# Optimization experiments

Measured on AMD Instinct MI355X. Metric: run time of the kernel, lower is better.

The kernel has to match this reference:

```python
import jax, jax.numpy as jnp
import numpy as np
from jax import lax

SIGMA, GAMMA, N_ORI = 6.0, 0.5, 6
WAVELENGTHS = (8.0, 10.0, 12.0)
KS = 37  # int(6*sigma)=36 -> +1 to make odd


def make_gabor_kernels():
    # Replicates cv2.getGaborKernel(psi=0); kernel is symmetric under 180-deg
    # rotation so cv2's index flip is a no-op and conv == correlation.
    half = KS // 2
    yy, xx = np.meshgrid(np.arange(-half, half + 1, dtype=np.float64),
                         np.arange(-half, half + 1, dtype=np.float64), indexing='ij')
    ks = []
    for lam in WAVELENGTHS:
        for t in range(N_ORI):
            th = t * np.pi / N_ORI
            xr = xx * np.cos(th) + yy * np.sin(th)
            yr = -xx * np.sin(th) + yy * np.cos(th)
            k = np.exp(-(xr ** 2 + (GAMMA ** 2) * yr ** 2) / (2.0 * SIGMA ** 2)) \
                * np.cos(2.0 * np.pi / lam * xr)
            ks.append(k.astype(np.float32))
    return jnp.asarray(np.stack(ks))[:, None]  # (F=18, 1, 37, 37)


def setup_inputs() -> dict:
    key = jax.random.key(0)
    x = jax.random.normal(key, (8, 3, 256, 256), dtype=jnp.float32)
    return {"x": x, "gabor_kernels": make_gabor_kernels()}


def haar_dwt2(x):
    # Single-level pywt haar dwt2; for even H,W symmetric padding never fires,
    # so each output pixel comes from a disjoint 2x2 block [[a,b],[c,d]].
    B, C, H, W = x.shape
    xb = x.reshape(B, C, H // 2, 2, W // 2, 2)
    a, b = xb[:, :, :, 0, :, 0], xb[:, :, :, 0, :, 1]
    c, d = xb[:, :, :, 1, :, 0], xb[:, :, :, 1, :, 1]
    LL = (a + b + c + d) * 0.5
    LH = (a + b - c - d) * 0.5  # pywt cH ('da'): high along rows
    HL = (a - b + c - d) * 0.5  # pywt cV ('ad'): high along cols
    HH = (a - b - c + d) * 0.5  # pywt cD ('dd')
    sub = jnp.stack([LL, LH, HL, HH], axis=2)  # (B, C, 4, H/2, W/2)
    return sub.reshape(B, C * 4, H // 2, W // 2)


def gabor_bank(x, kernels):
    # One grouped conv replaces the Python C x F conv2d loop. Group-major output
    # channel order (channel outer, filter inner) matches the torch loop order.
    B, C, H, W = x.shape
    F = kernels.shape[0]
    w = jnp.tile(kernels, (C, 1, 1, 1))  # (C*F, 1, KS, KS)
    pad = KS // 2
    return lax.conv_general_dilated(
        x, w, window_strides=(1, 1), padding=[(pad, pad), (pad, pad)],
        dimension_numbers=('NCHW', 'OIHW', 'NCHW'), feature_group_count=C)


def fft_channels(x):
    B, C, H, W = x.shape
    xc = jnp.fft.rfft2(x, norm='ortho')       # (B, C, H, W//2+1)
    mag = jnp.abs(xc)
    ph = jnp.arctan2(xc.imag, xc.real)        # torch.angle
    pad = W - mag.shape[-1]
    pads = [(0, 0), (0, 0), (0, 0), (0, pad)]
    return jnp.concatenate([jnp.pad(mag, pads), jnp.pad(ph, pads)], axis=1)


def reference(x, gabor_kernels):
    dwt = haar_dwt2(x)                 # (B, C*4, H/2, W/2)
    gab = gabor_bank(x, gabor_kernels)  # (B, C*18, H, W)
    fft = fft_channels(x)              # (B, C*2, H, W)
    return (dwt, gab, fft)
```

## Files before the change

### kernel.cpp

```cpp
#include <hip/hip_runtime.h>
#include <math.h>

#define BB 8
#define CC 3
#define HH 256
#define WW 256
#define KSZ 37
#define PD 18

#define DWT_OFF 0
#define GAB_OFF (8*12*128*128)
#define FFT_OFF (GAB_OFF + 8*54*256*256)

#define PSTRIDE 88

#define PREP_BLOCKS 888
#define FFTROW_BLOCKS 768
#define GAB_BLOCKS 1536
#define FFTCOL_BLOCKS 768

typedef short bf16x8 __attribute__((ext_vector_type(8)));
typedef float f32x16 __attribute__((ext_vector_type(16)));

__device__ __forceinline__ unsigned f2bf(float f) {
  unsigned u = __float_as_uint(f);
  return (u + 0x7fffu + ((u >> 16) & 1u)) >> 16;
}

__global__ __launch_bounds__(512) void fused_pre_kernel(
    const float* __restrict__ x, const float* __restrict__ wk,
    ushort* __restrict__ wshc, float* __restrict__ out) {
  __shared__ __align__(16) float smem[4352];
  const int g = blockIdx.x;
  const int tid = threadIdx.x;

  if (g < PREP_BLOCKS) {
    int idx = g * 512 + tid;
    int j = idx & 7; int rest = idx >> 3;
    int l = rest & 63; rest >>= 6;
    int t = rest % 3; rest /= 3;
    int ky = rest % 37; int s = rest / 37;
    int m = l & 31, hi = l >> 5;
    int kk = 16 * t + 8 * hi + j - s;
    float v = 0.0f;
    if (m < 18 && kk >= 0 && kk < 37) v = wk[(m * 37 + ky) * 37 + kk];
    wshc[idx] = (ushort)f2bf(v);
    return;
  }

  const int w = tid >> 6;
  const int t = tid & 63;
  const int rowid = (g - PREP_BLOCKS) * 8 + w;
  float* re  = smem + w * 256;
  float* im  = smem + 2048 + w * 256;
  float* twr = smem + 4096;
  float* twi = smem + 4224;

#pragma unroll
  for (int q = 0; q < 2; ++q) {
    int k = t + q * 64;
    float sn, cs;
    sincosf(-2.0f * (float)M_PI * (float)k / 256.0f, &sn, &cs);
    twr[k] = cs; twi[k] = sn;
  }

  const float* xr = x + (size_t)rowid * 256;
#pragma unroll
  for (int q = 0; q < 4; ++q) {
    int i = t + q * 64;
    int br = __brev((unsigned)i) >> 24;
    re[br] = xr[i];
    im[br] = 0.0f;
  }

  for (int s = 1; s <= 8; ++s) {
    int half = 1 << (s - 1);
    int sh = 8 - s;
#pragma unroll
    for (int q = 0; q < 2; ++q) {
      int j = t + q * 64;
      int gg = j >> (s - 1);
      int p = j & (half - 1);
      int i1 = (gg << s) + p;
      int i2 = i1 + half;
      float cs = twr[p << sh], sn = twi[p << sh];
      float r2 = re[i2], m2 = im[i2];
      float tr = r2 * cs - m2 * sn;
      float ti = r2 * sn + m2 * cs;
      float r1 = re[i1], m1 = im[i1];
      re[i2] = r1 - tr; im[i2] = m1 - ti;
      re[i1] = r1 + tr; im[i1] = m1 + ti;
    }
  }

  const int bc = rowid >> 8;
  const int y  = rowid & 255;
  const int b  = bc / 3, c = bc - b * 3;
  float* magrow = out + FFT_OFF + (size_t)(b * 6 + c) * (HH * WW) + (size_t)y * WW;
  float* phrow  = magrow + (size_t)3 * (HH * WW);
#pragma unroll
  for (int q = 0; q < 2; ++q) {
    int k = t + q * 64;
    magrow[k] = re[k];
    phrow[k]  = im[k];
  }
  if (t == 0) { magrow[128] = re[128]; phrow[128] = im[128]; }
}

#define LOAD_B_SET \
    r0 = *reinterpret_cast<const bf16x8*>(bp); \
    r1 = *reinterpret_cast<const bf16x8*>(bp + 8); \
    r2 = *reinterpret_cast<const bf16x8*>(bp + 16); \
    r3 = *reinterpret_cast<const bf16x8*>(bp + 24); \
    r4 = *reinterpret_cast<const bf16x8*>(bp + 32); \
    r5 = *reinterpret_cast<const bf16x8*>(bp + 40); \
    r6 = *reinterpret_cast<const bf16x8*>(bp + 48); \
    r7 = *reinterpret_cast<const bf16x8*>(bp + 56);
#define MFMA_GROUP(A0, A1, A2) \
    acc0 = __builtin_amdgcn_mfma_f32_32x32x16_bf16(A0, r0, acc0, 0, 0, 0); \
    acc1 = __builtin_amdgcn_mfma_f32_32x32x16_bf16(A0, r1, acc1, 0, 0, 0); \
    acc2 = __builtin_amdgcn_mfma_f32_32x32x16_bf16(A0, r2, acc2, 0, 0, 0); \
    acc3 = __builtin_amdgcn_mfma_f32_32x32x16_bf16(A0, r3, acc3, 0, 0, 0); \
    acc0 = __builtin_amdgcn_mfma_f32_32x32x16_bf16(A1, r2, acc0, 0, 0, 0); \
    acc1 = __builtin_amdgcn_mfma_f32_32x32x16_bf16(A1, r3, acc1, 0, 0, 0); \
    acc2 = __builtin_amdgcn_mfma_f32_32x32x16_bf16(A1, r4, acc2, 0, 0, 0); \
    acc3 = __builtin_amdgcn_mfma_f32_32x32x16_bf16(A1, r5, acc3, 0, 0, 0); \
    acc0 = __builtin_amdgcn_mfma_f32_32x32x16_bf16(A2, r4, acc0, 0, 0, 0); \
    acc1 = __builtin_amdgcn_mfma_f32_32x32x16_bf16(A2, r5, acc1, 0, 0, 0); \
    acc2 = __builtin_amdgcn_mfma_f32_32x32x16_bf16(A2, r6, acc2, 0, 0, 0); \
    acc3 = __builtin_amdgcn_mfma_f32_32x32x16_bf16(A2, r7, acc3, 0, 0, 0);

__global__ __launch_bounds__(512, 4) void fused_main_kernel(
    const float* __restrict__ x, const ushort* __restrict__ wshc,
    float* __restrict__ out) {
  __shared__ __align__(16) float smem[7216];
  const int g = blockIdx.x;
  const int tid = threadIdx.x;

  if (g < GAB_BLOCKS) {
    unsigned* patchU = reinterpret_cast<unsigned*>(smem);
    float* cbuf = smem + 2992;
    const int tile = g & 63;
    const int rest = g >> 6;
    const int cin = rest % 3, b = rest / 3;
    const int tileX = (tile & 7) * 32;
    const int tileY = (tile >> 3) * 32;
    const float* xp = x + (size_t)(b * CC + cin) * (HH * WW);

    for (int idx = tid; idx < 68 * (PSTRIDE / 2); idx += 512) {
      int r = idx / (PSTRIDE / 2), dc = idx - r * (PSTRIDE / 2);
      int gy = tileY + r - PD;
      int gx0 = tileX + 2 * dc - PD;
      float v0 = 0.0f, v1 = 0.0f;
      if ((unsigned)gy < 256u) {
        if ((unsigned)gx0 < 256u)       v0 = xp[gy * WW + gx0];
        if ((unsigned)(gx0 + 1) < 256u) v1 = xp[gy * WW + gx0 + 1];
      }
      patchU[idx] = f2bf(v0) | (f2bf(v1) << 16);
    }
    __syncthreads();

    const int w  = tid >> 6;
    const int l  = tid & 63;
    const int n  = l & 31;
    const int hi = l >> 5;

    f32x16 acc0 = {0.f,0.f,0.f,0.f,0.f,0.f,0.f,0.f,0.f,0.f,0.f,0.f,0.f,0.f,0.f,0.f};
    f32x16 acc1 = acc0, acc2 = acc0, acc3 = acc0;

    const ushort* patchS = reinterpret_cast<const ushort*>(patchU);
    const ushort* ap = wshc + (size_t)w * (37 * 3 * 512) + (size_t)l * 8;
    const ushort* bp = patchS + (size_t)n * PSTRIDE + hi * 8;

    bf16x8 aA0, aA1, aA2, aB0, aB1, aB2;
    bf16x8 r0, r1, r2, r3, r4, r5, r6, r7;

    aA0 = *reinterpret_cast<const bf16x8*>(ap);
    aA1 = *reinterpret_cast<const bf16x8*>(ap + 512);
    aA2 = *reinterpret_cast<const bf16x8*>(ap + 1024);

    for (int kp = 0; kp < 18; ++kp) {
      aB0 = *reinterpret_cast<const bf16x8*>(ap + 1536);
      aB1 = *reinterpret_cast<const bf16x8*>(ap + 2048);
      aB2 = *reinterpret_cast<const bf16x8*>(ap + 2560);
      LOAD_B_SET
      MFMA_GROUP(aA0, aA1, aA2)
      bp += PSTRIDE;
      aA0 = *reinterpret_cast<const bf16x8*>(ap + 3072);
      aA1 = *reinterpret_cast<const bf16x8*>(ap + 3584);
      aA2 = *reinterpret_cast<const bf16x8*>(ap + 4096);
      LOAD_B_SET
      MFMA_GROUP(aB0, aB1, aB2)
      ap += 3072;
      bp += PSTRIDE;
    }
    {
      LOAD_B_SET
      MFMA_GROUP(aA0, aA1, aA2)
    }
    __syncthreads();

    float* outb = out + GAB_OFF + (size_t)(b * 54 + cin * 18) * (HH * WW);
#pragma unroll
    for (int gq = 0; gq < 5; ++gq) {
      if (hi == (gq & 1)) {
        const int rq = gq >> 1;
#pragma unroll
        for (int q = 0; q < 4; ++q) {
          const int e = 4 * rq + q;
          float* crow = &cbuf[(q * 32 + n) * 33 + w];
          crow[0]  = acc0[e];
          crow[8]  = acc1[e];
          crow[16] = acc2[e];
          crow[24] = acc3[e];
        }
      }
      __syncthreads();
#pragma unroll
      for (int it = 0; it < 8; ++it) {
        int idx = tid + it * 512;
        int xo = idx & 31, yo = (idx >> 5) & 31, q = idx >> 10;
        int f = 4 * gq + q;
        if (f < 18)
          outb[(size_t)f * (HH * WW) + (size_t)(tileY + yo) * WW + tileX + xo] =
              cbuf[(q * 32 + yo) * 33 + xo];
      }
      __syncthreads();
    }
    return;
  }

  const int w = tid >> 6;
  const int t = tid & 63;
  const int colid = (g - GAB_BLOCKS) * 8 + w;
  const int bc = colid >> 8;
  const int k  = colid & 255;
  const int b  = bc / 3, c = bc - b * 3;
  float* re  = smem + w * 256;
  float* im  = smem + 2048 + w * 256;
  float* twr = smem + 4096;
  float* twi = smem + 4224;

#pragma unroll
  for (int q = 0; q < 2; ++q) {
    int kk = t + q * 64;
    float sn, cs;
    sincosf(-2.0f * (float)M_PI * (float)kk / 256.0f, &sn, &cs);
    twr[kk] = cs; twi[kk] = sn;
  }

  float* magp = out + FFT_OFF + (size_t)(b * 6 + c) * (HH * WW);
  float* php  = magp + (size_t)3 * (HH * WW);
  const bool live = (k < 129);
#pragma unroll
  for (int q = 0; q < 4; ++q) {
    int y = t + q * 64;
    int br = __brev((unsigned)y) >> 24;
    re[br] = live ? magp[(size_t)y * WW + k] : 0.0f;
    im[br] = live ? php[(size_t)y * WW + k]  : 0.0f;
  }

  for (int s = 1; s <= 8; ++s) {
    int half = 1 << (s - 1);
    int sh = 8 - s;
#pragma unroll
    for (int q = 0; q < 2; ++q) {
      int j = t + q * 64;
      int gg = j >> (s - 1);
      int p = j & (half - 1);
      int i1 = (gg << s) + p;
      int i2 = i1 + half;
      float cs = twr[p << sh], sn = twi[p << sh];
      float r2 = re[i2], m2 = im[i2];
      float tr = r2 * cs - m2 * sn;
      float ti = r2 * sn + m2 * cs;
      float r1 = re[i1], m1 = im[i1];
      re[i2] = r1 - tr; im[i2] = m1 - ti;
      re[i1] = r1 + tr; im[i1] = m1 + ti;
    }
  }

  const float scale = 1.0f / 256.0f;
#pragma unroll
  for (int q = 0; q < 4; ++q) {
    int u = t + q * 64;
    float r = re[u], m = im[u];
    magp[(size_t)u * WW + k] = sqrtf(r * r + m * m) * scale;
    php[(size_t)u * WW + k]  = atan2f(m, r);
  }
}

__global__ __launch_bounds__(256) void haar_dwt_kernel(
    const float* __restrict__ x, float* __restrict__ out) {
  int idx = blockIdx.x * 256 + threadIdx.x;
  if (idx >= BB * CC * 128 * 128) return;
  int j  = idx & 127;
  int i  = (idx >> 7) & 127;
  int bc = idx >> 14;
  const float* xp = x + (size_t)bc * (HH * WW);
  float2 top = *reinterpret_cast<const float2*>(&xp[(2 * i) * WW + 2 * j]);
  float2 bot = *reinterpret_cast<const float2*>(&xp[(2 * i + 1) * WW + 2 * j]);
  float a = top.x, b = top.y, c = bot.x, d = bot.y;
  int bI = bc / 3, cI = bc % 3;
  float* op = out + DWT_OFF + ((size_t)(bI * 12 + cI * 4) * 128 + i) * 128 + j;
  op[0]     = (a + b + c + d) * 0.5f;
  op[16384] = (a + b - c - d) * 0.5f;
  op[32768] = (a - b + c - d) * 0.5f;
  op[49152] = (a - b - c + d) * 0.5f;
}

extern "C" void kernel_launch(void* const* d_in, const int* in_sizes, int n_in,
                              void* d_out, int out_size, void* d_ws, size_t ws_size,
                              hipStream_t stream) {
  const float* x  = (const float*)d_in[0];
  const float* wk = (const float*)d_in[1];
  float* out = (float*)d_out;

  ushort* wshc = (ushort*)(out + DWT_OFF);

  fused_pre_kernel<<<dim3(PREP_BLOCKS + FFTROW_BLOCKS), dim3(512), 0, stream>>>(
      x, wk, wshc, out);
  fused_main_kernel<<<dim3(GAB_BLOCKS + FFTCOL_BLOCKS), dim3(512), 0, stream>>>(
      x, wshc, out);
  haar_dwt_kernel<<<dim3(1536), dim3(256), 0, stream>>>(x, out);
}
```

Baseline: 169.1 us.

## Fuse Haar DWT into main kernel and interleave block types

When a workspace is available, the packed bf16 Gabor weights move out of the DWT output region into the workspace. That lets the Haar DWT run as extra blocks inside the main kernel instead of as a separate third launch. Block indices are also interleaved, so each group of 4 holds 2 Gabor blocks, 1 FFT-column block and 1 DWT block, mixing compute-heavy and memory-heavy work on each CU. This removes one kernel launch and its tail, at the cost of an extra branch and a dependence on the workspace size.

```diff
diff --git a/kernel.cpp b/kernel.cpp
--- a/kernel.cpp
+++ b/kernel.cpp
@@ -18,6 +18,9 @@
 #define FFTROW_BLOCKS 768
 #define GAB_BLOCKS 1536
 #define FFTCOL_BLOCKS 768
+#define DWT_BLOCKS 768
+
+#define WSHC_BYTES (454656 * 2)
 
 typedef short bf16x8 __attribute__((ext_vector_type(8)));
 typedef float f32x16 __attribute__((ext_vector_type(16)));
@@ -132,16 +135,21 @@
 
 __global__ __launch_bounds__(512, 4) void fused_main_kernel(
     const float* __restrict__ x, const ushort* __restrict__ wshc,
-    float* __restrict__ out) {
+    float* __restrict__ out, int withDwt) {
   __shared__ __align__(16) float smem[7216];
   const int g = blockIdx.x;
   const int tid = threadIdx.x;
 
-  if (g < GAB_BLOCKS) {
+  int q4, r4;
+  if (withDwt) { q4 = g >> 2; r4 = g & 3; }
+  else         { q4 = g / 3;  r4 = g % 3; }
+
+  if (r4 < 2) {
+    const int gid = 2 * q4 + r4;
     unsigned* patchU = reinterpret_cast<unsigned*>(smem);
     float* cbuf = smem + 2992;
-    const int tile = g & 63;
-    const int rest = g >> 6;
+    const int tile = gid & 63;
+    const int rest = gid >> 6;
     const int cin = rest % 3, b = rest / 3;
     const int tileX = (tile & 7) * 32;
     const int tileY = (tile >> 3) * 32;
@@ -230,9 +238,27 @@
     return;
   }
 
+  if (r4 == 3) {
+    int idx = q4 * 512 + tid;
+    int j  = idx & 127;
+    int i  = (idx >> 7) & 127;
+    int bc = idx >> 14;
+    const float* xp = x + (size_t)bc * (HH * WW);
+    float2 top = *reinterpret_cast<const float2*>(&xp[(2 * i) * WW + 2 * j]);
+    float2 bot = *reinterpret_cast<const float2*>(&xp[(2 * i + 1) * WW + 2 * j]);
+    float a = top.x, bb = top.y, c = bot.x, d = bot.y;
+    int bI = bc / 3, cI = bc % 3;
+    float* op = out + DWT_OFF + ((size_t)(bI * 12 + cI * 4) * 128 + i) * 128 + j;
+    op[0]     = (a + bb + c + d) * 0.5f;
+    op[16384] = (a + bb - c - d) * 0.5f;
+    op[32768] = (a - bb + c - d) * 0.5f;
+    op[49152] = (a - bb - c + d) * 0.5f;
+    return;
+  }
+
   const int w = tid >> 6;
   const int t = tid & 63;
-  const int colid = (g - GAB_BLOCKS) * 8 + w;
+  const int colid = q4 * 8 + w;
   const int bc = colid >> 8;
   const int k  = colid & 255;
   const int b  = bc / 3, c = bc - b * 3;
@@ -316,11 +342,15 @@
   const float* wk = (const float*)d_in[1];
   float* out = (float*)d_out;
 
-  ushort* wshc = (ushort*)(out + DWT_OFF);
+  const bool ws_ok = (ws_size >= (size_t)WSHC_BYTES) && (d_ws != nullptr);
+  ushort* wshc = ws_ok ? (ushort*)d_ws : (ushort*)(out + DWT_OFF);
 
   fused_pre_kernel<<<dim3(PREP_BLOCKS + FFTROW_BLOCKS), dim3(512), 0, stream>>>(
       x, wk, wshc, out);
-  fused_main_kernel<<<dim3(GAB_BLOCKS + FFTCOL_BLOCKS), dim3(512), 0, stream>>>(
-      x, wshc, out);
-  haar_dwt_kernel<<<dim3(1536), dim3(256), 0, stream>>>(x, out);
-}
+  if (ws_ok) {
+    fused_main_kernel<<<dim3(4 * 768), dim3(512), 0, stream>>>(x, wshc, out, 1);
+  } else {
+    fused_main_kernel<<<dim3(3 * 768), dim3(512), 0, stream>>>(x, wshc, out, 0);
+    haar_dwt_kernel<<<dim3(1536), dim3(256), 0, stream>>>(x, out);
+  }
+}
```

Result: slower. 270.7 us (+60.1%).

## Widen Gabor MFMA tile to 64 columns with eight accumulators per wave

Applied to the files above, without the earlier changes.

The Gabor convolution tile grows from 32x32 to 32x64 output pixels, so each wave holds eight accumulator blocks instead of four. Each A-fragment (filter weights) load now feeds 24 MFMAs instead of 12, halving the weight traffic per output. The patch stride and shared buffer grow to fit, and the block count is halved. In exchange, register pressure doubles, which forces the occupancy hint down from 4 to 2 blocks per CU.

```diff
diff --git a/kernel.cpp b/kernel.cpp
--- a/kernel.cpp
+++ b/kernel.cpp
@@ -12,11 +12,11 @@
 #define GAB_OFF (8*12*128*128)
 #define FFT_OFF (GAB_OFF + 8*54*256*256)
 
-#define PSTRIDE 88
+#define PSTRIDE 120
 
 #define PREP_BLOCKS 888
 #define FFTROW_BLOCKS 768
-#define GAB_BLOCKS 1536
+#define GAB_BLOCKS 768
 #define FFTCOL_BLOCKS 768
 
 typedef short bf16x8 __attribute__((ext_vector_type(8)));
@@ -63,7 +63,6 @@
     sincosf(-2.0f * (float)M_PI * (float)k / 256.0f, &sn, &cs);
     twr[k] = cs; twi[k] = sn;
   }
-
   const float* xr = x + (size_t)rowid * 256;
 #pragma unroll
   for (int q = 0; q < 4; ++q) {
@@ -72,7 +71,6 @@
     re[br] = xr[i];
     im[br] = 0.0f;
   }
-
   for (int s = 1; s <= 8; ++s) {
     int half = 1 << (s - 1);
     int sh = 8 - s;
@@ -92,7 +90,6 @@
       re[i1] = r1 + tr; im[i1] = m1 + ti;
     }
   }
-
   const int bc = rowid >> 8;
   const int y  = rowid & 255;
   const int b  = bc / 3, c = bc - b * 3;
@@ -107,44 +104,60 @@
   if (t == 0) { magrow[128] = re[128]; phrow[128] = im[128]; }
 }
 
-#define LOAD_B_SET \
-    r0 = *reinterpret_cast<const bf16x8*>(bp); \
-    r1 = *reinterpret_cast<const bf16x8*>(bp + 8); \
-    r2 = *reinterpret_cast<const bf16x8*>(bp + 16); \
-    r3 = *reinterpret_cast<const bf16x8*>(bp + 24); \
-    r4 = *reinterpret_cast<const bf16x8*>(bp + 32); \
-    r5 = *reinterpret_cast<const bf16x8*>(bp + 40); \
-    r6 = *reinterpret_cast<const bf16x8*>(bp + 48); \
-    r7 = *reinterpret_cast<const bf16x8*>(bp + 56);
-#define MFMA_GROUP(A0, A1, A2) \
-    acc0 = __builtin_amdgcn_mfma_f32_32x32x16_bf16(A0, r0, acc0, 0, 0, 0); \
-    acc1 = __builtin_amdgcn_mfma_f32_32x32x16_bf16(A0, r1, acc1, 0, 0, 0); \
-    acc2 = __builtin_amdgcn_mfma_f32_32x32x16_bf16(A0, r2, acc2, 0, 0, 0); \
-    acc3 = __builtin_amdgcn_mfma_f32_32x32x16_bf16(A0, r3, acc3, 0, 0, 0); \
-    acc0 = __builtin_amdgcn_mfma_f32_32x32x16_bf16(A1, r2, acc0, 0, 0, 0); \
-    acc1 = __builtin_amdgcn_mfma_f32_32x32x16_bf16(A1, r3, acc1, 0, 0, 0); \
-    acc2 = __builtin_amdgcn_mfma_f32_32x32x16_bf16(A1, r4, acc2, 0, 0, 0); \
-    acc3 = __builtin_amdgcn_mfma_f32_32x32x16_bf16(A1, r5, acc3, 0, 0, 0); \
-    acc0 = __builtin_amdgcn_mfma_f32_32x32x16_bf16(A2, r4, acc0, 0, 0, 0); \
-    acc1 = __builtin_amdgcn_mfma_f32_32x32x16_bf16(A2, r5, acc1, 0, 0, 0); \
-    acc2 = __builtin_amdgcn_mfma_f32_32x32x16_bf16(A2, r6, acc2, 0, 0, 0); \
-    acc3 = __builtin_amdgcn_mfma_f32_32x32x16_bf16(A2, r7, acc3, 0, 0, 0);
-
-__global__ __launch_bounds__(512, 4) void fused_main_kernel(
+#define LOAD_B12 \
+    r0  = *reinterpret_cast<const bf16x8*>(bp); \
+    r1  = *reinterpret_cast<const bf16x8*>(bp + 8); \
+    r2  = *reinterpret_cast<const bf16x8*>(bp + 16); \
+    r3  = *reinterpret_cast<const bf16x8*>(bp + 24); \
+    r4  = *reinterpret_cast<const bf16x8*>(bp + 32); \
+    r5  = *reinterpret_cast<const bf16x8*>(bp + 40); \
+    r6  = *reinterpret_cast<const bf16x8*>(bp + 48); \
+    r7  = *reinterpret_cast<const bf16x8*>(bp + 56); \
+    r8  = *reinterpret_cast<const bf16x8*>(bp + 64); \
+    r9  = *reinterpret_cast<const bf16x8*>(bp + 72); \
+    r10 = *reinterpret_cast<const bf16x8*>(bp + 80); \
+    r11 = *reinterpret_cast<const bf16x8*>(bp + 88);
+#define MFMA24(A0, A1, A2) \
+    acc0 = __builtin_amdgcn_mfma_f32_32x32x16_bf16(A0, r0,  acc0, 0, 0, 0); \
+    acc1 = __builtin_amdgcn_mfma_f32_32x32x16_bf16(A0, r1,  acc1, 0, 0, 0); \
+    acc2 = __builtin_amdgcn_mfma_f32_32x32x16_bf16(A0, r2,  acc2, 0, 0, 0); \
+    acc3 = __builtin_amdgcn_mfma_f32_32x32x16_bf16(A0, r3,  acc3, 0, 0, 0); \
+    acc4 = __builtin_amdgcn_mfma_f32_32x32x16_bf16(A0, r4,  acc4, 0, 0, 0); \
+    acc5 = __builtin_amdgcn_mfma_f32_32x32x16_bf16(A0, r5,  acc5, 0, 0, 0); \
+    acc6 = __builtin_amdgcn_mfma_f32_32x32x16_bf16(A0, r6,  acc6, 0, 0, 0); \
+    acc7 = __builtin_amdgcn_mfma_f32_32x32x16_bf16(A0, r7,  acc7, 0, 0, 0); \
+    acc0 = __builtin_amdgcn_mfma_f32_32x32x16_bf16(A1, r2,  acc0, 0, 0, 0); \
+    acc1 = __builtin_amdgcn_mfma_f32_32x32x16_bf16(A1, r3,  acc1, 0, 0, 0); \
+    acc2 = __builtin_amdgcn_mfma_f32_32x32x16_bf16(A1, r4,  acc2, 0, 0, 0); \
+    acc3 = __builtin_amdgcn_mfma_f32_32x32x16_bf16(A1, r5,  acc3, 0, 0, 0); \
+    acc4 = __builtin_amdgcn_mfma_f32_32x32x16_bf16(A1, r6,  acc4, 0, 0, 0); \
+    acc5 = __builtin_amdgcn_mfma_f32_32x32x16_bf16(A1, r7,  acc5, 0, 0, 0); \
+    acc6 = __builtin_amdgcn_mfma_f32_32x32x16_bf16(A1, r8,  acc6, 0, 0, 0); \
+    acc7 = __builtin_amdgcn_mfma_f32_32x32x16_bf16(A1, r9,  acc7, 0, 0, 0); \
+    acc0 = __builtin_amdgcn_mfma_f32_32x32x16_bf16(A2, r4,  acc0, 0, 0, 0); \
+    acc1 = __builtin_amdgcn_mfma_f32_32x32x16_bf16(A2, r5,  acc1, 0, 0, 0); \
+    acc2 = __builtin_amdgcn_mfma_f32_32x32x16_bf16(A2, r6,  acc2, 0, 0, 0); \
+    acc3 = __builtin_amdgcn_mfma_f32_32x32x16_bf16(A2, r7,  acc3, 0, 0, 0); \
+    acc4 = __builtin_amdgcn_mfma_f32_32x32x16_bf16(A2, r8,  acc4, 0, 0, 0); \
+    acc5 = __builtin_amdgcn_mfma_f32_32x32x16_bf16(A2, r9,  acc5, 0, 0, 0); \
+    acc6 = __builtin_amdgcn_mfma_f32_32x32x16_bf16(A2, r10, acc6, 0, 0, 0); \
+    acc7 = __builtin_amdgcn_mfma_f32_32x32x16_bf16(A2, r11, acc7, 0, 0, 0);
+
+__global__ __launch_bounds__(512, 2) void fused_main_kernel(
     const float* __restrict__ x, const ushort* __restrict__ wshc,
     float* __restrict__ out) {
-  __shared__ __align__(16) float smem[7216];
+  __shared__ __align__(16) float smem[8320];
   const int g = blockIdx.x;
   const int tid = threadIdx.x;
 
   if (g < GAB_BLOCKS) {
     unsigned* patchU = reinterpret_cast<unsigned*>(smem);
-    float* cbuf = smem + 2992;
-    const int tile = g & 63;
-    const int rest = g >> 6;
-    const int cin = rest % 3, b = rest / 3;
-    const int tileX = (tile & 7) * 32;
-    const int tileY = (tile >> 3) * 32;
+    const int xt  = g & 3;
+    const int yt  = (g >> 2) & 7;
+    const int img = g >> 5;
+    const int cin = img % 3, b = img / 3;
+    const int tileX = xt * 64;
+    const int tileY = yt * 32;
     const float* xp = x + (size_t)(b * CC + cin) * (HH * WW);
 
     for (int idx = tid; idx < 68 * (PSTRIDE / 2); idx += 512) {
@@ -167,63 +180,69 @@
 
     f32x16 acc0 = {0.f,0.f,0.f,0.f,0.f,0.f,0.f,0.f,0.f,0.f,0.f,0.f,0.f,0.f,0.f,0.f};
     f32x16 acc1 = acc0, acc2 = acc0, acc3 = acc0;
+    f32x16 acc4 = acc0, acc5 = acc0, acc6 = acc0, acc7 = acc0;
 
     const ushort* patchS = reinterpret_cast<const ushort*>(patchU);
     const ushort* ap = wshc + (size_t)w * (37 * 3 * 512) + (size_t)l * 8;
     const ushort* bp = patchS + (size_t)n * PSTRIDE + hi * 8;
 
     bf16x8 aA0, aA1, aA2, aB0, aB1, aB2;
-    bf16x8 r0, r1, r2, r3, r4, r5, r6, r7;
+    bf16x8 r0, r1, r2, r3, r4, r5, r6, r7, r8, r9, r10, r11;
 
     aA0 = *reinterpret_cast<const bf16x8*>(ap);
     aA1 = *reinterpret_cast<const bf16x8*>(ap + 512);
     aA2 = *reinterpret_cast<const bf16x8*>(ap + 1024);
 
     for (int kp = 0; kp < 18; ++kp) {
+      LOAD_B12
       aB0 = *reinterpret_cast<const bf16x8*>(ap + 1536);
       aB1 = *reinterpret_cast<const bf16x8*>(ap + 2048);
       aB2 = *reinterpret_cast<const bf16x8*>(ap + 2560);
-      LOAD_B_SET
-      MFMA_GROUP(aA0, aA1, aA2)
+      MFMA24(aA0, aA1, aA2)
       bp += PSTRIDE;
+      LOAD_B12
       aA0 = *reinterpret_cast<const bf16x8*>(ap + 3072);
       aA1 = *reinterpret_cast<const bf16x8*>(ap + 3584);
       aA2 = *reinterpret_cast<const bf16x8*>(ap + 4096);
-      LOAD_B_SET
-      MFMA_GROUP(aB0, aB1, aB2)
+      MFMA24(aB0, aB1, aB2)
       ap += 3072;
       bp += PSTRIDE;
     }
     {
-      LOAD_B_SET
-      MFMA_GROUP(aA0, aA1, aA2)
+      LOAD_B12
+      MFMA24(aA0, aA1, aA2)
     }
     __syncthreads();
 
+    float* cbuf = smem;
     float* outb = out + GAB_OFF + (size_t)(b * 54 + cin * 18) * (HH * WW);
 #pragma unroll
     for (int gq = 0; gq < 5; ++gq) {
       if (hi == (gq & 1)) {
         const int rq = gq >> 1;
 #pragma unroll
-        for (int q = 0; q < 4; ++q) {
-          const int e = 4 * rq + q;
-          float* crow = &cbuf[(q * 32 + n) * 33 + w];
+        for (int fq = 0; fq < 4; ++fq) {
+          const int e = 4 * rq + fq;
+          float* crow = &cbuf[(fq * 32 + n) * 65 + w];
           crow[0]  = acc0[e];
           crow[8]  = acc1[e];
           crow[16] = acc2[e];
           crow[24] = acc3[e];
+          crow[32] = acc4[e];
+          crow[40] = acc5[e];
+          crow[48] = acc6[e];
+          crow[56] = acc7[e];
         }
       }
       __syncthreads();
 #pragma unroll
-      for (int it = 0; it < 8; ++it) {
+      for (int it = 0; it < 16; ++it) {
         int idx = tid + it * 512;
-        int xo = idx & 31, yo = (idx >> 5) & 31, q = idx >> 10;
-        int f = 4 * gq + q;
+        int xo = idx & 63, yo = (idx >> 6) & 31, fq = idx >> 11;
+        int f = 4 * gq + fq;
         if (f < 18)
           outb[(size_t)f * (HH * WW) + (size_t)(tileY + yo) * WW + tileX + xo] =
-              cbuf[(q * 32 + yo) * 33 + xo];
+              cbuf[(fq * 32 + yo) * 65 + xo];
       }
       __syncthreads();
     }
```

New measurement: 179.1 us. 1.06x slower.

## Pack gabor filter-shift rows densely into five waves per tile

Applied to the files above, without the earlier changes.

Repacks the im2col weight matrix so the 144 real filter×shift rows fill 5 waves of 32 rows, instead of 8 waves that each computed 14 padded dummy rows. The main kernel drops to 320 threads, with a matching epilogue that remaps each accumulator row to its filter and shift, and the column FFT is re-split to 5 columns per block. This cuts wasted MFMA work and LDS/weight loads, at the cost of more complex index math in the epilogue and fewer threads for patch loading and stores.

```diff
diff --git a/kernel.cpp b/kernel.cpp
--- a/kernel.cpp
+++ b/kernel.cpp
@@ -13,11 +13,12 @@
 #define FFT_OFF (GAB_OFF + 8*54*256*256)
 
 #define PSTRIDE 88
-
-#define PREP_BLOCKS 888
+#define WROLE_SZ (37*3*512)
+
+#define PREP_BLOCKS 555
 #define FFTROW_BLOCKS 768
 #define GAB_BLOCKS 1536
-#define FFTCOL_BLOCKS 768
+#define FFTCOL_BLOCKS 1229
 
 typedef short bf16x8 __attribute__((ext_vector_type(8)));
 typedef float f32x16 __attribute__((ext_vector_type(16)));
@@ -36,14 +37,21 @@
 
   if (g < PREP_BLOCKS) {
     int idx = g * 512 + tid;
-    int j = idx & 7; int rest = idx >> 3;
-    int l = rest & 63; rest >>= 6;
+    int e = idx & 7;
+    int l = (idx >> 3) & 63;
+    int rest = idx >> 9;
     int t = rest % 3; rest /= 3;
-    int ky = rest % 37; int s = rest / 37;
+    int ky = rest % 37;
+    int w = rest / 37;
     int m = l & 31, hi = l >> 5;
-    int kk = 16 * t + 8 * hi + j - s;
+    int p = 32 * w + m;
     float v = 0.0f;
-    if (m < 18 && kk >= 0 && kk < 37) v = wk[(m * 37 + ky) * 37 + kk];
+    if (p < 144) {
+      int s = p / 18;
+      int f = p - 18 * s;
+      int kk = 16 * t + 8 * hi + e - s;
+      if (kk >= 0 && kk < 37) v = wk[(f * 37 + ky) * 37 + kk];
+    }
     wshc[idx] = (ushort)f2bf(v);
     return;
   }
@@ -63,7 +71,6 @@
     sincosf(-2.0f * (float)M_PI * (float)k / 256.0f, &sn, &cs);
     twr[k] = cs; twi[k] = sn;
   }
-
   const float* xr = x + (size_t)rowid * 256;
 #pragma unroll
   for (int q = 0; q < 4; ++q) {
@@ -72,7 +79,6 @@
     re[br] = xr[i];
     im[br] = 0.0f;
   }
-
   for (int s = 1; s <= 8; ++s) {
     int half = 1 << (s - 1);
     int sh = 8 - s;
@@ -92,7 +98,6 @@
       re[i1] = r1 + tr; im[i1] = m1 + ti;
     }
   }
-
   const int bc = rowid >> 8;
   const int y  = rowid & 255;
   const int b  = bc / 3, c = bc - b * 3;
@@ -130,16 +135,15 @@
     acc2 = __builtin_amdgcn_mfma_f32_32x32x16_bf16(A2, r6, acc2, 0, 0, 0); \
     acc3 = __builtin_amdgcn_mfma_f32_32x32x16_bf16(A2, r7, acc3, 0, 0, 0);
 
-__global__ __launch_bounds__(512, 4) void fused_main_kernel(
+__global__ __launch_bounds__(320, 4) void fused_main_kernel(
     const float* __restrict__ x, const ushort* __restrict__ wshc,
     float* __restrict__ out) {
-  __shared__ __align__(16) float smem[7216];
+  __shared__ __align__(16) float smem[4224];
   const int g = blockIdx.x;
   const int tid = threadIdx.x;
 
   if (g < GAB_BLOCKS) {
     unsigned* patchU = reinterpret_cast<unsigned*>(smem);
-    float* cbuf = smem + 2992;
     const int tile = g & 63;
     const int rest = g >> 6;
     const int cin = rest % 3, b = rest / 3;
@@ -147,7 +151,7 @@
     const int tileY = (tile >> 3) * 32;
     const float* xp = x + (size_t)(b * CC + cin) * (HH * WW);
 
-    for (int idx = tid; idx < 68 * (PSTRIDE / 2); idx += 512) {
+    for (int idx = tid; idx < 68 * (PSTRIDE / 2); idx += 320) {
       int r = idx / (PSTRIDE / 2), dc = idx - r * (PSTRIDE / 2);
       int gy = tileY + r - PD;
       int gx0 = tileX + 2 * dc - PD;
@@ -169,7 +173,7 @@
     f32x16 acc1 = acc0, acc2 = acc0, acc3 = acc0;
 
     const ushort* patchS = reinterpret_cast<const ushort*>(patchU);
-    const ushort* ap = wshc + (size_t)w * (37 * 3 * 512) + (size_t)l * 8;
+    const ushort* ap = wshc + (size_t)w * WROLE_SZ + (size_t)l * 8;
     const ushort* bp = patchS + (size_t)n * PSTRIDE + hi * 8;
 
     bf16x8 aA0, aA1, aA2, aB0, aB1, aB2;
@@ -200,30 +204,37 @@
     }
     __syncthreads();
 
+    float* cbuf = smem;
     float* outb = out + GAB_OFF + (size_t)(b * 54 + cin * 18) * (HH * WW);
 #pragma unroll
     for (int gq = 0; gq < 5; ++gq) {
-      if (hi == (gq & 1)) {
-        const int rq = gq >> 1;
-#pragma unroll
-        for (int q = 0; q < 4; ++q) {
-          const int e = 4 * rq + q;
-          float* crow = &cbuf[(q * 32 + n) * 33 + w];
-          crow[0]  = acc0[e];
-          crow[8]  = acc1[e];
-          crow[16] = acc2[e];
-          crow[24] = acc3[e];
+#pragma unroll
+      for (int e = 0; e < 16; ++e) {
+        int m = (e & 3) + 8 * (e >> 2) + 4 * hi;
+        int p = 32 * w + m;
+        if (p < 144) {
+          int s = p / 18;
+          int f = p - 18 * s;
+          if ((f >> 2) == gq) {
+            float* crow = &cbuf[((f & 3) * 32 + n) * 33 + s];
+            crow[0]  = acc0[e];
+            crow[8]  = acc1[e];
+            crow[16] = acc2[e];
+            crow[24] = acc3[e];
+          }
         }
       }
       __syncthreads();
 #pragma unroll
-      for (int it = 0; it < 8; ++it) {
-        int idx = tid + it * 512;
-        int xo = idx & 31, yo = (idx >> 5) & 31, q = idx >> 10;
-        int f = 4 * gq + q;
-        if (f < 18)
-          outb[(size_t)f * (HH * WW) + (size_t)(tileY + yo) * WW + tileX + xo] =
-              cbuf[(q * 32 + yo) * 33 + xo];
+      for (int it = 0; it < 13; ++it) {
+        int idx = tid + it * 320;
+        if (idx < 4096) {
+          int xo = idx & 31, yo = (idx >> 5) & 31, fq = idx >> 10;
+          int f = 4 * gq + fq;
+          if (f < 18)
+            outb[(size_t)f * (HH * WW) + (size_t)(tileY + yo) * WW + tileX + xo] =
+                cbuf[(fq * 32 + yo) * 33 + xo];
+        }
       }
       __syncthreads();
     }
@@ -232,14 +243,15 @@
 
   const int w = tid >> 6;
   const int t = tid & 63;
-  const int colid = (g - GAB_BLOCKS) * 8 + w;
+  const int colid = (g - GAB_BLOCKS) * 5 + w;
+  if (colid >= 6144) return;
   const int bc = colid >> 8;
   const int k  = colid & 255;
   const int b  = bc / 3, c = bc - b * 3;
-  float* re  = smem + w * 256;
-  float* im  = smem + 2048 + w * 256;
-  float* twr = smem + 4096;
-  float* twi = smem + 4224;
+  float* re  = smem + w * 512;
+  float* im  = smem + w * 512 + 256;
+  float* twr = smem + 2560;
+  float* twi = smem + 2688;
 
 #pragma unroll
   for (int q = 0; q < 2; ++q) {
@@ -320,7 +332,7 @@
 
   fused_pre_kernel<<<dim3(PREP_BLOCKS + FFTROW_BLOCKS), dim3(512), 0, stream>>>(
       x, wk, wshc, out);
-  fused_main_kernel<<<dim3(GAB_BLOCKS + FFTCOL_BLOCKS), dim3(512), 0, stream>>>(
+  fused_main_kernel<<<dim3(GAB_BLOCKS + FFTCOL_BLOCKS), dim3(320), 0, stream>>>(
       x, wshc, out);
   haar_dwt_kernel<<<dim3(1536), dim3(256), 0, stream>>>(x, out);
 }
```

After: 169.8 us. Within noise of the previous version (+0.4%).
